# Optimization experiments

Hardware: AMD Instinct MI355X
Metric: run time of the kernel (lower is better)

Reference implementation:

```python
import jax, jax.numpy as jnp
import numpy as np

B, N, M, C = 2, 16384, 16, 64
D_HIDDEN = 64  # int(d * hidden_scale) with d=64, hidden_scale=1
BN_EPS = 1e-5


def setup_inputs() -> dict:
    key = jax.random.key(0)
    ks = jax.random.split(key, 10)
    s = 1.0 / np.sqrt(C)
    return {
        "center_feat": jax.random.normal(ks[0], (B, N, C), jnp.float32),
        "neighbor_feat": jax.random.normal(ks[1], (B, N, M, C), jnp.float32),
        "pos_enc": jax.random.normal(ks[2], (B, N, M, C), jnp.float32),
        "Wq": jax.random.normal(ks[3], (C, C), jnp.float32) * s,      # nn.Linear(d, d), no bias
        "Wkv": jax.random.normal(ks[4], (2 * C, C), jnp.float32) * s, # nn.Linear(d, 2d), no bias
        "W1": jax.random.normal(ks[5], (D_HIDDEN, C), jnp.float32) * s,  # 1x1 Conv2d(d, d_hidden)
        "bn_gamma": jnp.ones((D_HIDDEN,), jnp.float32),
        "bn_beta": jnp.zeros((D_HIDDEN,), jnp.float32),
        "bn_mean": jax.random.normal(ks[6], (D_HIDDEN,), jnp.float32) * 0.1,
        "bn_var": jax.random.uniform(ks[7], (D_HIDDEN,), jnp.float32, 0.5, 1.5),
        "W2": jax.random.normal(ks[8], (C, D_HIDDEN), jnp.float32) * (1.0 / np.sqrt(D_HIDDEN)),  # 1x1 Conv2d(d_hidden, d)
    }


def reference(center_feat, neighbor_feat, pos_enc, Wq, Wkv, W1, bn_gamma, bn_beta, bn_mean, bn_var, W2):
    # Q = Linear(center_feat): (B, N, C)
    Q = jnp.einsum("bnc,dc->bnd", center_feat, Wq)
    # K, V = chunk(Linear(neighbor_feat), 2): each (B, N, M, C)
    KV = jnp.einsum("bnmc,dc->bnmd", neighbor_feat, Wkv)
    K, V = jnp.split(KV, 2, axis=-1)
    # broadcast subtract + pos enc: (B, N, M, C)
    attn = Q[:, :, None, :] - K + pos_enc
    # mlp: 1x1 conv -> BN (eval, running stats) -> ReLU -> 1x1 conv (channel = last axis)
    h = jnp.einsum("bnmc,hc->bnmh", attn, W1)
    h = (h - bn_mean) * (bn_gamma / jnp.sqrt(bn_var + BN_EPS)) + bn_beta
    h = jax.nn.relu(h)
    attn = jnp.einsum("bnmh,ch->bnmc", h, W2)
    # softmax over neighbor dim M, weighted sum
    w = jax.nn.softmax(attn, axis=2)
    return jnp.sum(w * (V + pos_enc), axis=2)  # (B, N, C)
```

## Files before the change

### kernel.cpp

```cpp
#include <hip/hip_runtime.h>
#include <hip/hip_bf16.h>
#include <stdint.h>


#define NN 16384

typedef float f32x4 __attribute__((ext_vector_type(4)));
typedef short s16x8 __attribute__((ext_vector_type(8)));
typedef int   i32x4 __attribute__((ext_vector_type(4)));

__device__ __forceinline__ uint32_t pk2(float a, float b) {
  float2 f; f.x = a; f.y = b;
  __hip_bfloat162 h = __float22bfloat162_rn(f);
  uint32_t u;
  __builtin_memcpy(&u, &h, 4);
  return u;
}

__device__ __forceinline__ f32x4 mma16(i32x4 a, i32x4 b, f32x4 c) {
  return __builtin_amdgcn_mfma_f32_16x16x32_bf16(
      __builtin_bit_cast(s16x8, a), __builtin_bit_cast(s16x8, b), c, 0, 0, 0);
}

__device__ __forceinline__ i32x4 packfrag(f32x4 f0, f32x4 f1) {
  i32x4 r;
  r.x = pk2(f0.x, f0.y); r.y = pk2(f0.z, f0.w);
  r.z = pk2(f1.x, f1.y); r.w = pk2(f1.z, f1.w);
  return r;
}

__device__ __forceinline__ void wstore(uint16_t* wp, int mat, int j, int k, float v) {
  int ct = j >> 4, jl = j & 15;
  int kt = k >> 5, r = k & 31;
  int kh = r >> 4, rr = r & 15;
  int gg = rr >> 2, e2 = rr & 3;
  int lanei = jl + (gg << 4);
  int e = kh * 4 + e2;
  uint32_t u = __builtin_bit_cast(uint32_t, v);
  u += 0x7fffu + ((u >> 16) & 1u);
  wp[((mat * 8 + kt * 4 + ct) * 64 + lanei) * 8 + e] = (uint16_t)(u >> 16);
}

__global__ void prep_weights(const float* __restrict__ Wq, const float* __restrict__ Wkv,
                             const float* __restrict__ W1, const float* __restrict__ gam,
                             const float* __restrict__ bet, const float* __restrict__ mu,
                             const float* __restrict__ var, const float* __restrict__ W2,
                             uint16_t* __restrict__ wp, float* __restrict__ b1) {
  int j = blockIdx.x * 16 + (threadIdx.x >> 4);
  int q = threadIdx.x & 15;
  float gp = gam[j] * rsqrtf(var[j] + 1e-5f);
  if (q == 0) b1[j] = bet[j] - gp * mu[j];
  for (int k = q * 4; k < q * 4 + 4; ++k) {
    float aq = 0.f, ak = 0.f;
    for (int c = 0; c < 64; ++c) {
      float w1 = W1[j * 64 + c];
      aq += w1 * Wq[c * 64 + k];
      ak += w1 * Wkv[c * 64 + k];
    }
    wstore(wp, 0, j, k, gp * aq);
    wstore(wp, 1, j, k, -gp * ak);
    wstore(wp, 2, j, k, gp * W1[j * 64 + k]);
    wstore(wp, 3, j, k, Wkv[(64 + j) * 64 + k]);
    wstore(wp, 4, j, k, W2[j * 64 + k]);
  }
}

#define W_LDS_ELEMS (4 * 4096)

__device__ __forceinline__ i32x4 bfragld(const uint16_t* wlds, int mat, int kt, int ct, int lane) {
  return *(const i32x4*)(wlds + ((mat * 8 + kt * 4 + ct) * 64 + lane) * 8);
}

__global__ __launch_bounds__(256, 2) void vattn_main(
    const float* __restrict__ center, const float* __restrict__ nbr,
    const float* __restrict__ pos, const uint16_t* __restrict__ wp,
    const float* __restrict__ b1, float* __restrict__ out) {
  __shared__ uint16_t wlds[W_LDS_ELEMS];
  const int tid = threadIdx.x;
  {
    const i32x4* src = (const i32x4*)wp;
    i32x4* dst = (i32x4*)wlds;
#pragma unroll
    for (int i = 0; i < 8; ++i) dst[tid + 256 * i] = src[tid + 256 * i];
  }

  const int w = tid >> 6;
  const int lane = tid & 63;
  const int l15 = lane & 15;
  const int g = lane >> 4;

  i32x4 w2f[2][4];
#pragma unroll
  for (int kt = 0; kt < 2; ++kt)
#pragma unroll
    for (int ct = 0; ct < 4; ++ct)
      w2f[kt][ct] = *(const i32x4*)(wp + ((32 + kt * 4 + ct) * 64 + lane) * 8);

  f32x4 binit[4];
#pragma unroll
  for (int ct = 0; ct < 4; ++ct)
#pragma unroll
    for (int r = 0; r < 4; ++r) binit[ct][r] = b1[ct * 16 + 4 * g + r];

  __syncthreads();

  const int blk = blockIdx.x;
  const int b = blk >> 9;
  const int n0 = (blk & 511) << 5;
  const long nbase = (long)b * NN + n0 + (w << 3);

  f32x4 rn[2][4], rp[2][4], rc[2][4];

#define ISSUE(BUF, RT) do {                                                    \
    const long nr_ = nbase + (RT);                                             \
    const float* nrp_ = nbr + ((nr_ * 16 + l15) * 64) + g * 4;                 \
    const float* prp_ = pos + ((nr_ * 16 + l15) * 64) + g * 4;                 \
    const float* crp_ = center + nr_ * 64 + g * 4;                             \
    rn[BUF][0] = *(const f32x4*)nrp_;        rn[BUF][1] = *(const f32x4*)(nrp_ + 16); \
    rn[BUF][2] = *(const f32x4*)(nrp_ + 32); rn[BUF][3] = *(const f32x4*)(nrp_ + 48); \
    rp[BUF][0] = *(const f32x4*)prp_;        rp[BUF][1] = *(const f32x4*)(prp_ + 16); \
    rp[BUF][2] = *(const f32x4*)(prp_ + 32); rp[BUF][3] = *(const f32x4*)(prp_ + 48); \
    rc[BUF][0] = *(const f32x4*)crp_;        rc[BUF][1] = *(const f32x4*)(crp_ + 16); \
    rc[BUF][2] = *(const f32x4*)(crp_ + 32); rc[BUF][3] = *(const f32x4*)(crp_ + 48); \
    __builtin_amdgcn_sched_barrier(0);                                         \
  } while (0)

  ISSUE(0, 0);

#pragma unroll
  for (int rt = 0; rt < 8; ++rt) {
    if (rt < 7) ISSUE((rt + 1) & 1, rt + 1);
    const int buf = rt & 1;
    const long nrow = nbase + rt;

    const float* pr = pos + nrow * 1024;
    f32x4 rq[4];
#pragma unroll
    for (int ct = 0; ct < 4; ++ct)
#pragma unroll
      for (int r = 0; r < 4; ++r)
        rq[ct][r] = pr[(4 * g + r) * 64 + ct * 16 + l15];

    i32x4 na0 = packfrag(rn[buf][0], rn[buf][1]);
    i32x4 na1 = packfrag(rn[buf][2], rn[buf][3]);
    i32x4 pa0 = packfrag(rp[buf][0], rp[buf][1]);
    i32x4 pa1 = packfrag(rp[buf][2], rp[buf][3]);
    i32x4 ca0 = packfrag(rc[buf][0], rc[buf][1]);
    i32x4 ca1 = packfrag(rc[buf][2], rc[buf][3]);

    f32x4 h[4];
#pragma unroll
    for (int ct = 0; ct < 4; ++ct) {
      h[ct] = binit[ct];
      h[ct] = mma16(bfragld(wlds, 0, 0, ct, lane), ca0, h[ct]);
      h[ct] = mma16(bfragld(wlds, 0, 1, ct, lane), ca1, h[ct]);
      h[ct] = mma16(bfragld(wlds, 1, 0, ct, lane), na0, h[ct]);
      h[ct] = mma16(bfragld(wlds, 1, 1, ct, lane), na1, h[ct]);
      h[ct] = mma16(bfragld(wlds, 2, 0, ct, lane), pa0, h[ct]);
      h[ct] = mma16(bfragld(wlds, 2, 1, ct, lane), pa1, h[ct]);
    }

    f32x4 vv[4];
#pragma unroll
    for (int ct = 0; ct < 4; ++ct) {
      vv[ct] = rq[ct];
      vv[ct] = mma16(na0, bfragld(wlds, 3, 0, ct, lane), vv[ct]);
      vv[ct] = mma16(na1, bfragld(wlds, 3, 1, ct, lane), vv[ct]);
    }

    i32x4 ha0, ha1;
    {
      f32x4 r0, r1, r2, r3;
#pragma unroll
      for (int r = 0; r < 4; ++r) {
        r0[r] = fmaxf(h[0][r], 0.f); r1[r] = fmaxf(h[1][r], 0.f);
        r2[r] = fmaxf(h[2][r], 0.f); r3[r] = fmaxf(h[3][r], 0.f);
      }
      ha0 = packfrag(r0, r1);
      ha1 = packfrag(r2, r3);
    }

    f32x4 a2[4];
#pragma unroll
    for (int ct = 0; ct < 4; ++ct) {
      a2[ct] = (f32x4){0.f, 0.f, 0.f, 0.f};
      a2[ct] = mma16(ha0, w2f[0][ct], a2[ct]);
      a2[ct] = mma16(ha1, w2f[1][ct], a2[ct]);
    }

    float ov[4];
#pragma unroll
    for (int ct = 0; ct < 4; ++ct) {
      f32x4 s = a2[ct];
      float mx = fmaxf(fmaxf(s.x, s.y), fmaxf(s.z, s.w));
      mx = fmaxf(mx, __shfl_xor(mx, 16, 64));
      mx = fmaxf(mx, __shfl_xor(mx, 32, 64));
      float e0 = __expf(s.x - mx), e1 = __expf(s.y - mx);
      float e2 = __expf(s.z - mx), e3 = __expf(s.w - mx);
      float sm = e0 + e1 + e2 + e3;
      sm += __shfl_xor(sm, 16, 64);
      sm += __shfl_xor(sm, 32, 64);
      float ps = e0 * vv[ct].x + e1 * vv[ct].y + e2 * vv[ct].z + e3 * vv[ct].w;
      ps += __shfl_xor(ps, 16, 64);
      ps += __shfl_xor(ps, 32, 64);
      ov[ct] = ps * __builtin_amdgcn_rcpf(sm);
    }
    float val = (g == 0) ? ov[0] : (g == 1) ? ov[1] : (g == 2) ? ov[2] : ov[3];
    out[nrow * 64 + lane] = val;
  }
#undef ISSUE
}

extern "C" void kernel_launch(void* const* d_in, const int* in_sizes, int n_in,
                              void* d_out, int out_size, void* d_ws, size_t ws_size,
                              hipStream_t stream) {
  const float* center = (const float*)d_in[0];
  const float* nbr    = (const float*)d_in[1];
  const float* pos    = (const float*)d_in[2];
  const float* Wq     = (const float*)d_in[3];
  const float* Wkv    = (const float*)d_in[4];
  const float* W1     = (const float*)d_in[5];
  const float* gam    = (const float*)d_in[6];
  const float* bet    = (const float*)d_in[7];
  const float* mu     = (const float*)d_in[8];
  const float* var    = (const float*)d_in[9];
  const float* W2     = (const float*)d_in[10];
  uint16_t* wp = (uint16_t*)d_ws;
  float* b1 = (float*)((char*)d_ws + 5 * 4096 * 2);
  prep_weights<<<4, 256, 0, stream>>>(Wq, Wkv, W1, gam, bet, mu, var, W2, wp, b1);
  vattn_main<<<1024, 256, 0, stream>>>(center, nbr, pos, wp, b1, (float*)d_out);
}
```

Measured before the change: 101.7 us.

## Stage neighbor and pos tiles via async global-to-LDS ring buffer

Replaces register double-buffered global loads of neighbor and pos rows with a per-wave two-slot LDS ring filled by global_load_lds, prefetching two rows ahead with explicit vmcnt waits. The transposed pos read for V+pos now comes from LDS instead of a second strided global read. To free LDS for the ring, the W1 and Wv weight fragments move from LDS into registers. This raises register pressure and LDS use (64KB ring plus 16KB weights), which may lower occupancy below the two-blocks-per-CU launch bound.

```diff
diff --git a/kernel.cpp b/kernel.cpp
--- a/kernel.cpp
+++ b/kernel.cpp
@@ -4,6 +4,7 @@
 
 
 #define NN 16384
+#define RING_F 2048
 
 typedef float f32x4 __attribute__((ext_vector_type(4)));
 typedef short s16x8 __attribute__((ext_vector_type(8)));
@@ -65,8 +66,6 @@
   }
 }
 
-#define W_LDS_ELEMS (4 * 4096)
-
 __device__ __forceinline__ i32x4 bfragld(const uint16_t* wlds, int mat, int kt, int ct, int lane) {
   return *(const i32x4*)(wlds + ((mat * 8 + kt * 4 + ct) * 64 + lane) * 8);
 }
@@ -75,13 +74,14 @@
     const float* __restrict__ center, const float* __restrict__ nbr,
     const float* __restrict__ pos, const uint16_t* __restrict__ wp,
     const float* __restrict__ b1, float* __restrict__ out) {
-  __shared__ uint16_t wlds[W_LDS_ELEMS];
+  __shared__ uint16_t wlds[2 * 4096];
+  __shared__ float ring[4 * 2 * RING_F];
   const int tid = threadIdx.x;
   {
     const i32x4* src = (const i32x4*)wp;
     i32x4* dst = (i32x4*)wlds;
 #pragma unroll
-    for (int i = 0; i < 8; ++i) dst[tid + 256 * i] = src[tid + 256 * i];
+    for (int i = 0; i < 4; ++i) dst[tid + 256 * i] = src[tid + 256 * i];
   }
 
   const int w = tid >> 6;
@@ -89,12 +89,15 @@
   const int l15 = lane & 15;
   const int g = lane >> 4;
 
-  i32x4 w2f[2][4];
+  i32x4 a1f[2][4], wvf[2][4], w2f[2][4];
 #pragma unroll
   for (int kt = 0; kt < 2; ++kt)
 #pragma unroll
-    for (int ct = 0; ct < 4; ++ct)
+    for (int ct = 0; ct < 4; ++ct) {
+      a1f[kt][ct] = *(const i32x4*)(wp + ((16 + kt * 4 + ct) * 64 + lane) * 8);
+      wvf[kt][ct] = *(const i32x4*)(wp + ((24 + kt * 4 + ct) * 64 + lane) * 8);
       w2f[kt][ct] = *(const i32x4*)(wp + ((32 + kt * 4 + ct) * 64 + lane) * 8);
+    }
 
   f32x4 binit[4];
 #pragma unroll
@@ -108,45 +111,64 @@
   const int b = blk >> 9;
   const int n0 = (blk & 511) << 5;
   const long nbase = (long)b * NN + n0 + (w << 3);
-
-  f32x4 rn[2][4], rp[2][4], rc[2][4];
-
-#define ISSUE(BUF, RT) do {                                                    \
-    const long nr_ = nbase + (RT);                                             \
-    const float* nrp_ = nbr + ((nr_ * 16 + l15) * 64) + g * 4;                 \
-    const float* prp_ = pos + ((nr_ * 16 + l15) * 64) + g * 4;                 \
-    const float* crp_ = center + nr_ * 64 + g * 4;                             \
-    rn[BUF][0] = *(const f32x4*)nrp_;        rn[BUF][1] = *(const f32x4*)(nrp_ + 16); \
-    rn[BUF][2] = *(const f32x4*)(nrp_ + 32); rn[BUF][3] = *(const f32x4*)(nrp_ + 48); \
-    rp[BUF][0] = *(const f32x4*)prp_;        rp[BUF][1] = *(const f32x4*)(prp_ + 16); \
-    rp[BUF][2] = *(const f32x4*)(prp_ + 32); rp[BUF][3] = *(const f32x4*)(prp_ + 48); \
-    rc[BUF][0] = *(const f32x4*)crp_;        rc[BUF][1] = *(const f32x4*)(crp_ + 16); \
-    rc[BUF][2] = *(const f32x4*)(crp_ + 32); rc[BUF][3] = *(const f32x4*)(crp_ + 48); \
-    __builtin_amdgcn_sched_barrier(0);                                         \
+  float* myring = ring + w * 2 * RING_F;
+
+#define STAGE(SLOT, NR) do {                                                   \
+    const float* gn_ = nbr + (long)(NR) * 1024 + lane * 4;                     \
+    const float* gp_ = pos + (long)(NR) * 1024 + lane * 4;                     \
+    float* l_ = myring + (SLOT) * RING_F;                                      \
+    _Pragma("unroll")                                                          \
+    for (int c_ = 0; c_ < 4; ++c_) {                                           \
+      __builtin_amdgcn_global_load_lds(                                        \
+          (const __attribute__((address_space(1))) void*)(gn_ + c_ * 256),     \
+          (__attribute__((address_space(3))) void*)(l_ + c_ * 256), 16, 0, 0); \
+      __builtin_amdgcn_global_load_lds(                                        \
+          (const __attribute__((address_space(1))) void*)(gp_ + c_ * 256),     \
+          (__attribute__((address_space(3))) void*)(l_ + 1024 + c_ * 256), 16, 0, 0); \
+    }                                                                          \
   } while (0)
 
-  ISSUE(0, 0);
+  f32x4 cc[2][4];
+#define CCLOAD(BUF, NR) do {                                                   \
+    const float* crp_ = center + (long)(NR) * 64 + g * 4;                      \
+    cc[BUF][0] = *(const f32x4*)crp_;        cc[BUF][1] = *(const f32x4*)(crp_ + 16); \
+    cc[BUF][2] = *(const f32x4*)(crp_ + 32); cc[BUF][3] = *(const f32x4*)(crp_ + 48); \
+  } while (0)
+
+  STAGE(0, nbase);
+  CCLOAD(0, nbase);
+  STAGE(1, nbase + 1);
 
 #pragma unroll
   for (int rt = 0; rt < 8; ++rt) {
-    if (rt < 7) ISSUE((rt + 1) & 1, rt + 1);
-    const int buf = rt & 1;
-    const long nrow = nbase + rt;
-
-    const float* pr = pos + nrow * 1024;
+    const int slot = rt & 1;
+    if (rt == 7) asm volatile("s_waitcnt vmcnt(0)" ::: "memory");
+    else         asm volatile("s_waitcnt vmcnt(8)" ::: "memory");
+
+    const float* dn = myring + slot * RING_F;
+    const float* dp = dn + 1024;
+    const float* nb_ = dn + l15 * 64 + g * 4;
+    f32x4 rn0 = *(const f32x4*)nb_,        rn1 = *(const f32x4*)(nb_ + 16);
+    f32x4 rn2 = *(const f32x4*)(nb_ + 32), rn3 = *(const f32x4*)(nb_ + 48);
+    const float* pb_ = dp + l15 * 64 + g * 4;
+    f32x4 rp0 = *(const f32x4*)pb_,        rp1 = *(const f32x4*)(pb_ + 16);
+    f32x4 rp2 = *(const f32x4*)(pb_ + 32), rp3 = *(const f32x4*)(pb_ + 48);
     f32x4 rq[4];
 #pragma unroll
     for (int ct = 0; ct < 4; ++ct)
 #pragma unroll
       for (int r = 0; r < 4; ++r)
-        rq[ct][r] = pr[(4 * g + r) * 64 + ct * 16 + l15];
-
-    i32x4 na0 = packfrag(rn[buf][0], rn[buf][1]);
-    i32x4 na1 = packfrag(rn[buf][2], rn[buf][3]);
-    i32x4 pa0 = packfrag(rp[buf][0], rp[buf][1]);
-    i32x4 pa1 = packfrag(rp[buf][2], rp[buf][3]);
-    i32x4 ca0 = packfrag(rc[buf][0], rc[buf][1]);
-    i32x4 ca1 = packfrag(rc[buf][2], rc[buf][3]);
+        rq[ct][r] = dp[(4 * g + r) * 64 + ct * 16 + l15];
+    asm volatile("s_waitcnt lgkmcnt(0)" ::: "memory");
+    __builtin_amdgcn_sched_barrier(0);
+
+    if (rt + 1 < 8) CCLOAD((rt + 1) & 1, nbase + rt + 1);
+    if (rt + 2 < 8) STAGE(slot, nbase + rt + 2);
+
+    i32x4 na0 = packfrag(rn0, rn1), na1 = packfrag(rn2, rn3);
+    i32x4 pa0 = packfrag(rp0, rp1), pa1 = packfrag(rp2, rp3);
+    i32x4 ca0 = packfrag(cc[slot][0], cc[slot][1]);
+    i32x4 ca1 = packfrag(cc[slot][2], cc[slot][3]);
 
     f32x4 h[4];
 #pragma unroll
@@ -156,16 +178,16 @@
       h[ct] = mma16(bfragld(wlds, 0, 1, ct, lane), ca1, h[ct]);
       h[ct] = mma16(bfragld(wlds, 1, 0, ct, lane), na0, h[ct]);
       h[ct] = mma16(bfragld(wlds, 1, 1, ct, lane), na1, h[ct]);
-      h[ct] = mma16(bfragld(wlds, 2, 0, ct, lane), pa0, h[ct]);
-      h[ct] = mma16(bfragld(wlds, 2, 1, ct, lane), pa1, h[ct]);
+      h[ct] = mma16(a1f[0][ct], pa0, h[ct]);
+      h[ct] = mma16(a1f[1][ct], pa1, h[ct]);
     }
 
     f32x4 vv[4];
 #pragma unroll
     for (int ct = 0; ct < 4; ++ct) {
       vv[ct] = rq[ct];
-      vv[ct] = mma16(na0, bfragld(wlds, 3, 0, ct, lane), vv[ct]);
-      vv[ct] = mma16(na1, bfragld(wlds, 3, 1, ct, lane), vv[ct]);
+      vv[ct] = mma16(na0, wvf[0][ct], vv[ct]);
+      vv[ct] = mma16(na1, wvf[1][ct], vv[ct]);
     }
 
     i32x4 ha0, ha1;
@@ -188,6 +210,7 @@
       a2[ct] = mma16(ha1, w2f[1][ct], a2[ct]);
     }
 
+    const long nrow = nbase + rt;
     float ov[4];
 #pragma unroll
     for (int ct = 0; ct < 4; ++ct) {
@@ -208,7 +231,8 @@
     float val = (g == 0) ? ov[0] : (g == 1) ? ov[1] : (g == 2) ? ov[2] : ov[3];
     out[nrow * 64 + lane] = val;
   }
-#undef ISSUE
+#undef STAGE
+#undef CCLOAD
 }
 
 extern "C" void kernel_launch(void* const* d_in, const int* in_sizes, int n_in,
```

Measured after the change: 97.59 us. 1.04x faster.
